# Performance work log

Hardware: AMD Instinct MI355X
Metric: run time of the kernel (lower is better)

## Reference

```python
import jax, jax.numpy as jnp
import numpy as np

FP8_MAX = 448.0   # E4M3 max finite value
AMAX_EPS = 1e-8
MOMENTUM = 0.95


def _compute_scale(amax):
    return FP8_MAX / jnp.clip(amax, AMAX_EPS)


def _fp8_cast_ste(t, scale):
    """clamp(t*scale, +-448) -> fp8_e4m3 -> back to t.dtype, /scale. STE grad."""
    s = scale.astype(jnp.float32)
    t_scaled = jnp.clip(t.astype(jnp.float32) * s, -FP8_MAX, FP8_MAX)
    t_deq = t_scaled.astype(jnp.float8_e4m3fn).astype(t.dtype) / s.astype(t.dtype)
    # straight-through: forward value = t_deq, gradient = identity wrt t
    return t + jax.lax.stop_gradient(t_deq - t)


def _update_amax(buf, new_amax):
    new_amax = jnp.nan_to_num(new_amax, nan=AMAX_EPS, posinf=FP8_MAX, neginf=AMAX_EPS)
    return jnp.clip(jnp.maximum(buf * MOMENTUM, new_amax), AMAX_EPS)


def setup_inputs() -> dict:
    key = jax.random.key(0)
    k1, k2, k3 = jax.random.split(key, 3)
    x = jax.random.normal(k1, (8192, 4096), dtype=jnp.float32)
    weight = jax.random.normal(k2, (4096, 4096), dtype=jnp.float32) * 0.02
    bias = jax.random.normal(k3, (4096,), dtype=jnp.float32) * 0.01
    input_amax = jnp.ones((), dtype=jnp.float32)
    weight_amax = jnp.ones((), dtype=jnp.float32)
    return {"x": x, "weight": weight, "bias": bias,
            "input_amax": input_amax, "weight_amax": weight_amax}


def reference(x, weight, bias, input_amax, weight_amax):
    # delayed scaling: scales from previous-step amax buffers
    x_scale = _compute_scale(input_amax).astype(jnp.float32)
    w_scale = _compute_scale(weight_amax).astype(jnp.float32)
    x2 = x.reshape(-1, weight.shape[1])  # [T, in]
    x_q = _fp8_cast_ste(x2, x_scale)
    w_q = _fp8_cast_ste(weight, w_scale)
    out = jnp.einsum('ti,oi->to', x_q, w_q) + bias  # [T, out]
    # amax EMA updates (buffers)
    new_input_amax = _update_amax(input_amax, jnp.max(jnp.abs(x2)))
    new_weight_amax = _update_amax(weight_amax, jnp.max(jnp.abs(weight)))
    return out, new_input_amax, new_weight_amax
```

## Files before the change

### kernel.cpp

```cpp
#include <hip/hip_runtime.h>
#include <cstdint>
#include <cstddef>

#define FP8_MAXV 448.0f
#define AMAX_EPS 1e-8f
#define MOMENTUM 0.95f

#define M_DIM 8192
#define N_DIM 4096
#define K_DIM 4096

#define XBLOCKS 2048
#define WBLOCKS 1024

#define SCALE_ONE 0x7F7F7F7F

typedef float f32x4 __attribute__((ext_vector_type(4)));
typedef int   i32x4 __attribute__((ext_vector_type(4)));
typedef int   i32x8 __attribute__((ext_vector_type(8)));

__device__ __forceinline__ void gload_lds16(const void* g, void* l) {
  __builtin_amdgcn_global_load_lds(
      (const __attribute__((address_space(1))) void*)g,
      (__attribute__((address_space(3))) void*)l, 16, 0, 0);
}

__global__ __launch_bounds__(256) void k_quant(
    const float* __restrict__ x, const float* __restrict__ w,
    unsigned int* __restrict__ xq, unsigned int* __restrict__ wq,
    const float* __restrict__ ax_buf, const float* __restrict__ aw_buf,
    float* __restrict__ xpart, float* __restrict__ wpart) {
  const float* in;
  unsigned int* outq;
  float* part;
  int bid, nblocks, n4;
  float sc;
  if (blockIdx.x < XBLOCKS) {
    in = x; outq = xq; part = xpart;
    bid = blockIdx.x; nblocks = XBLOCKS; n4 = (M_DIM * K_DIM) / 4;
    sc = FP8_MAXV / fmaxf(ax_buf[0], AMAX_EPS);
  } else {
    in = w; outq = wq; part = wpart;
    bid = blockIdx.x - XBLOCKS; nblocks = WBLOCKS; n4 = (N_DIM * K_DIM) / 4;
    sc = FP8_MAXV / fmaxf(aw_buf[0], AMAX_EPS);
  }
  float lm = 0.0f;
  const int stride = nblocks * 256;
  for (int i = bid * 256 + threadIdx.x; i < n4; i += stride) {
    float4 v = ((const float4*)in)[i];
    lm = fmaxf(lm, fmaxf(fmaxf(fabsf(v.x), fabsf(v.y)),
                         fmaxf(fabsf(v.z), fabsf(v.w))));
    float a0 = fminf(fmaxf(v.x * sc, -FP8_MAXV), FP8_MAXV);
    float a1 = fminf(fmaxf(v.y * sc, -FP8_MAXV), FP8_MAXV);
    float a2 = fminf(fmaxf(v.z * sc, -FP8_MAXV), FP8_MAXV);
    float a3 = fminf(fmaxf(v.w * sc, -FP8_MAXV), FP8_MAXV);
    int p = 0;
    p = __builtin_amdgcn_cvt_pk_fp8_f32(a0, a1, p, false);
    p = __builtin_amdgcn_cvt_pk_fp8_f32(a2, a3, p, true);
    outq[i] = (unsigned int)p;
  }
  #pragma unroll
  for (int off = 32; off > 0; off >>= 1)
    lm = fmaxf(lm, __shfl_down(lm, off));
  __shared__ float smax[4];
  if ((threadIdx.x & 63) == 0) smax[threadIdx.x >> 6] = lm;
  __syncthreads();
  if (threadIdx.x == 0)
    part[bid] = fmaxf(fmaxf(smax[0], smax[1]), fmaxf(smax[2], smax[3]));
}

__global__ __launch_bounds__(256, 2) void k_gemm(
    const unsigned char* __restrict__ Aq, const unsigned char* __restrict__ Bq,
    const float* __restrict__ bias,
    const float* __restrict__ ax_buf, const float* __restrict__ aw_buf,
    const float* __restrict__ xpart, const float* __restrict__ wpart,
    float* __restrict__ out) {
  __shared__ __align__(16) unsigned char ldsA[128 * 128];
  __shared__ __align__(16) unsigned char ldsB[128 * 128];

  const int tid = threadIdx.x;
  const int w = tid >> 6;
  const int l = tid & 63;
  const int m = l & 15;
  const int q = l >> 4;
  const int wr = (w >> 1) * 64;
  const int wc = (w & 1) * 64;
  const int blockRow = blockIdx.y * 128;
  const int blockCol = blockIdx.x * 128;

  const int srow = l >> 3;
  const int sgrp = (l & 7) ^ srow;
  const unsigned char* gA =
      Aq + (size_t)(blockRow + w * 32 + srow) * K_DIM + sgrp * 16;
  const unsigned char* gB =
      Bq + (size_t)(blockCol + w * 32 + srow) * K_DIM + sgrp * 16;
  unsigned char* lA = &ldsA[w * 4096];
  unsigned char* lB = &ldsB[w * 4096];

  const int mk = m & 7;
  f32x4 acc[4][4] = {};

  for (int k0 = 0; k0 < K_DIM; k0 += 128) {
    #pragma unroll
    for (int cc = 0; cc < 4; ++cc) {
      gload_lds16(gA + k0 + (size_t)(cc * 8) * K_DIM, lA + cc * 1024);
      gload_lds16(gB + k0 + (size_t)(cc * 8) * K_DIM, lB + cc * 1024);
    }
    __syncthreads();

    i32x8 a[4], b[4];
    #pragma unroll
    for (int i = 0; i < 4; ++i) {
      const unsigned char* p = ldsA + (wr + i * 16 + m) * 128;
      i32x4 lo = *(const i32x4*)(p + (((2 * q) ^ mk) * 16));
      i32x4 hi = *(const i32x4*)(p + (((2 * q + 1) ^ mk) * 16));
      a[i] = __builtin_shufflevector(lo, hi, 0, 1, 2, 3, 4, 5, 6, 7);
    }
    #pragma unroll
    for (int j = 0; j < 4; ++j) {
      const unsigned char* p = ldsB + (wc + j * 16 + m) * 128;
      i32x4 lo = *(const i32x4*)(p + (((2 * q) ^ mk) * 16));
      i32x4 hi = *(const i32x4*)(p + (((2 * q + 1) ^ mk) * 16));
      b[j] = __builtin_shufflevector(lo, hi, 0, 1, 2, 3, 4, 5, 6, 7);
    }
    #pragma unroll
    for (int i = 0; i < 4; ++i)
      #pragma unroll
      for (int j = 0; j < 4; ++j)
        acc[i][j] = __builtin_amdgcn_mfma_scale_f32_16x16x128_f8f6f4(
            a[i], b[j], acc[i][j],  0,  0,
             0, SCALE_ONE,  0, SCALE_ONE);
    __syncthreads();
  }

  const float inv = fmaxf(ax_buf[0], AMAX_EPS) * fmaxf(aw_buf[0], AMAX_EPS) *
                    (1.0f / (FP8_MAXV * FP8_MAXV));

  #pragma unroll
  for (int j = 0; j < 4; ++j) {
    const int colg = blockCol + wc + j * 16 + m;
    const float bv = bias[colg];
    #pragma unroll
    for (int i = 0; i < 4; ++i) {
      const int rowg = blockRow + wr + i * 16 + q * 4;
      #pragma unroll
      for (int r = 0; r < 4; ++r)
        out[(size_t)(rowg + r) * N_DIM + colg] = acc[i][j][r] * inv + bv;
    }
  }

  if (blockIdx.x == 0 && blockIdx.y == 0) {
    float mx = 0.0f, mw = 0.0f;
    for (int i = tid; i < XBLOCKS; i += 256) mx = fmaxf(mx, xpart[i]);
    for (int i = tid; i < WBLOCKS; i += 256) mw = fmaxf(mw, wpart[i]);
    #pragma unroll
    for (int off = 32; off > 0; off >>= 1) {
      mx = fmaxf(mx, __shfl_down(mx, off));
      mw = fmaxf(mw, __shfl_down(mw, off));
    }
    __syncthreads();
    float* red = (float*)ldsA;
    if (l == 0) { red[w] = mx; red[4 + w] = mw; }
    __syncthreads();
    if (tid == 0) {
      mx = fmaxf(fmaxf(red[0], red[1]), fmaxf(red[2], red[3]));
      mw = fmaxf(fmaxf(red[4], red[5]), fmaxf(red[6], red[7]));
      float* tail = out + (size_t)M_DIM * N_DIM;
      tail[0] = fmaxf(fmaxf(ax_buf[0] * MOMENTUM, mx), AMAX_EPS);
      tail[1] = fmaxf(fmaxf(aw_buf[0] * MOMENTUM, mw), AMAX_EPS);
    }
  }
}

extern "C" void kernel_launch(void* const* d_in, const int* in_sizes, int n_in,
                              void* d_out, int out_size, void* d_ws, size_t ws_size,
                              hipStream_t stream) {
  const float* x      = (const float*)d_in[0];
  const float* weight = (const float*)d_in[1];
  const float* bias   = (const float*)d_in[2];
  const float* in_ax  = (const float*)d_in[3];
  const float* in_aw  = (const float*)d_in[4];
  float* out = (float*)d_out;

  float* xpart = (float*)d_ws;
  float* wpart = xpart + XBLOCKS;
  unsigned char* xq = (unsigned char*)d_ws + 16384;
  unsigned char* wq = xq + (size_t)M_DIM * K_DIM;

  k_quant<<<XBLOCKS + WBLOCKS, 256, 0, stream>>>(
      x, weight, (unsigned int*)xq, (unsigned int*)wq, in_ax, in_aw,
      xpart, wpart);

  dim3 grid(N_DIM / 128, M_DIM / 128);
  k_gemm<<<grid, 256, 0, stream>>>(xq, wq, bias, in_ax, in_aw,
                                   xpart, wpart, out);
}
```

Baseline: 408.3 us.

## Enlarge GEMM tile to 256x256 with double-buffered LDS and interleaved MFMA

The FP8 GEMM goes from a 128x128 tile with 4 waves to a 256x256 tile with 8 waves, each wave computing 128x64. LDS is double buffered so the next K-slab's global-to-LDS loads are issued before the current slab's MFMAs run. Fragment reads are interleaved with MFMA pairs under s_setprio. This aims to raise operand reuse and hide load latency behind compute, at the cost of 128KB of LDS per block and heavy register pressure from 32 accumulators, which may limit occupancy.

```diff
diff --git a/kernel.cpp b/kernel.cpp
--- a/kernel.cpp
+++ b/kernel.cpp
@@ -69,68 +69,110 @@
     part[bid] = fmaxf(fmaxf(smax[0], smax[1]), fmaxf(smax[2], smax[3]));
 }
 
-__global__ __launch_bounds__(256, 2) void k_gemm(
+__global__ __launch_bounds__(512, 2) void k_gemm(
     const unsigned char* __restrict__ Aq, const unsigned char* __restrict__ Bq,
     const float* __restrict__ bias,
     const float* __restrict__ ax_buf, const float* __restrict__ aw_buf,
     const float* __restrict__ xpart, const float* __restrict__ wpart,
     float* __restrict__ out) {
-  __shared__ __align__(16) unsigned char ldsA[128 * 128];
-  __shared__ __align__(16) unsigned char ldsB[128 * 128];
+  __shared__ __align__(16) unsigned char ldsA[2][256 * 128];
+  __shared__ __align__(16) unsigned char ldsB[2][256 * 128];
 
   const int tid = threadIdx.x;
   const int w = tid >> 6;
   const int l = tid & 63;
   const int m = l & 15;
   const int q = l >> 4;
-  const int wr = (w >> 1) * 64;
-  const int wc = (w & 1) * 64;
-  const int blockRow = blockIdx.y * 128;
-  const int blockCol = blockIdx.x * 128;
+  const int mk = m & 7;
+  const int wr = (w >> 2) * 128;
+  const int wc = (w & 3) * 64;
+  const int blockRow = blockIdx.y * 256;
+  const int blockCol = blockIdx.x * 256;
+
+  const int xlo = ((2 * q) ^ mk) * 16;
+  const int xhi = ((2 * q + 1) ^ mk) * 16;
 
   const int srow = l >> 3;
-  const int sgrp = (l & 7) ^ srow;
-  const unsigned char* gA =
-      Aq + (size_t)(blockRow + w * 32 + srow) * K_DIM + sgrp * 16;
-  const unsigned char* gB =
-      Bq + (size_t)(blockCol + w * 32 + srow) * K_DIM + sgrp * 16;
-  unsigned char* lA = &ldsA[w * 4096];
-  unsigned char* lB = &ldsB[w * 4096];
-
-  const int mk = m & 7;
-  f32x4 acc[4][4] = {};
-
-  for (int k0 = 0; k0 < K_DIM; k0 += 128) {
+  const int sgrp = ((l & 7) ^ srow) * 16;
+  const unsigned char* gA = Aq + (size_t)(blockRow + w * 32 + srow) * K_DIM + sgrp;
+  const unsigned char* gB = Bq + (size_t)(blockCol + w * 32 + srow) * K_DIM + sgrp;
+
+#define STAGE(bufidx, k0)                                              \
+  { _Pragma("unroll") for (int s = 0; s < 4; ++s) {                    \
+      gload_lds16(gA + (k0) + (size_t)(s * 8) * K_DIM,                 \
+                  &ldsA[bufidx][w * 4096 + s * 1024]);                 \
+      gload_lds16(gB + (k0) + (size_t)(s * 8) * K_DIM,                 \
+                  &ldsB[bufidx][w * 4096 + s * 1024]);                 \
+  } }
+
+#define FRAG2(lo, hi, off)                                             \
+  __builtin_shufflevector(*(const i32x4*)((lo) + (off)),               \
+                          *(const i32x4*)((hi) + (off)), 0, 1, 2, 3, 4, 5, 6, 7)
+
+#define MFMA_PAIR(i0, aX, aY)                                          \
+  { __builtin_amdgcn_s_setprio(1);                                     \
+    _Pragma("unroll") for (int j = 0; j < 4; ++j) {                    \
+      acc[(i0)][j] = __builtin_amdgcn_mfma_scale_f32_16x16x128_f8f6f4( \
+          aX, b[j], acc[(i0)][j], 0, 0, 0, SCALE_ONE, 0, SCALE_ONE);   \
+      acc[(i0) + 1][j] = __builtin_amdgcn_mfma_scale_f32_16x16x128_f8f6f4( \
+          aY, b[j], acc[(i0) + 1][j], 0, 0, 0, SCALE_ONE, 0, SCALE_ONE);   \
+    }                                                                  \
+    __builtin_amdgcn_s_setprio(0); }
+
+  f32x4 acc[8][4] = {};
+  const int NT = K_DIM / 128;
+
+  STAGE(0, 0);
+  asm volatile("s_waitcnt vmcnt(0)" ::: "memory");
+  __builtin_amdgcn_s_barrier();
+
+  i32x8 b[4], a0f, a1f;
+  {
+    const unsigned char* Blo = &ldsB[0][(wc + m) * 128 + xlo];
+    const unsigned char* Bhi = &ldsB[0][(wc + m) * 128 + xhi];
+    const unsigned char* Alo = &ldsA[0][(wr + m) * 128 + xlo];
+    const unsigned char* Ahi = &ldsA[0][(wr + m) * 128 + xhi];
     #pragma unroll
-    for (int cc = 0; cc < 4; ++cc) {
-      gload_lds16(gA + k0 + (size_t)(cc * 8) * K_DIM, lA + cc * 1024);
-      gload_lds16(gB + k0 + (size_t)(cc * 8) * K_DIM, lB + cc * 1024);
-    }
-    __syncthreads();
-
-    i32x8 a[4], b[4];
-    #pragma unroll
-    for (int i = 0; i < 4; ++i) {
-      const unsigned char* p = ldsA + (wr + i * 16 + m) * 128;
-      i32x4 lo = *(const i32x4*)(p + (((2 * q) ^ mk) * 16));
-      i32x4 hi = *(const i32x4*)(p + (((2 * q + 1) ^ mk) * 16));
-      a[i] = __builtin_shufflevector(lo, hi, 0, 1, 2, 3, 4, 5, 6, 7);
-    }
-    #pragma unroll
-    for (int j = 0; j < 4; ++j) {
-      const unsigned char* p = ldsB + (wc + j * 16 + m) * 128;
-      i32x4 lo = *(const i32x4*)(p + (((2 * q) ^ mk) * 16));
-      i32x4 hi = *(const i32x4*)(p + (((2 * q + 1) ^ mk) * 16));
-      b[j] = __builtin_shufflevector(lo, hi, 0, 1, 2, 3, 4, 5, 6, 7);
-    }
-    #pragma unroll
-    for (int i = 0; i < 4; ++i)
+    for (int j = 0; j < 4; ++j) b[j] = FRAG2(Blo, Bhi, j * 2048);
+    a0f = FRAG2(Alo, Ahi, 0);
+    a1f = FRAG2(Alo, Ahi, 2048);
+  }
+
+  for (int kt = 0; kt < NT; ++kt) {
+    const int cur = kt & 1;
+    const unsigned char* Alo = &ldsA[cur][(wr + m) * 128 + xlo];
+    const unsigned char* Ahi = &ldsA[cur][(wr + m) * 128 + xhi];
+
+    if (kt + 1 < NT) STAGE(cur ^ 1, (kt + 1) * 128);
+    MFMA_PAIR(0, a0f, a1f);
+    i32x8 a2f = FRAG2(Alo, Ahi, 2 * 2048);
+    i32x8 a3f = FRAG2(Alo, Ahi, 3 * 2048);
+    __builtin_amdgcn_s_barrier();
+
+    MFMA_PAIR(2, a2f, a3f);
+    i32x8 a4f = FRAG2(Alo, Ahi, 4 * 2048);
+    i32x8 a5f = FRAG2(Alo, Ahi, 5 * 2048);
+    __builtin_amdgcn_s_barrier();
+
+    MFMA_PAIR(4, a4f, a5f);
+    i32x8 a6f = FRAG2(Alo, Ahi, 6 * 2048);
+    i32x8 a7f = FRAG2(Alo, Ahi, 7 * 2048);
+    asm volatile("s_waitcnt vmcnt(0)" ::: "memory");
+    __builtin_amdgcn_s_barrier();
+
+    MFMA_PAIR(6, a6f, a7f);
+    if (kt + 1 < NT) {
+      const int nxt = cur ^ 1;
+      const unsigned char* Bnlo = &ldsB[nxt][(wc + m) * 128 + xlo];
+      const unsigned char* Bnhi = &ldsB[nxt][(wc + m) * 128 + xhi];
+      const unsigned char* Anlo = &ldsA[nxt][(wr + m) * 128 + xlo];
+      const unsigned char* Anhi = &ldsA[nxt][(wr + m) * 128 + xhi];
       #pragma unroll
-      for (int j = 0; j < 4; ++j)
-        acc[i][j] = __builtin_amdgcn_mfma_scale_f32_16x16x128_f8f6f4(
-            a[i], b[j], acc[i][j],  0,  0,
-             0, SCALE_ONE,  0, SCALE_ONE);
-    __syncthreads();
+      for (int j = 0; j < 4; ++j) b[j] = FRAG2(Bnlo, Bnhi, j * 2048);
+      a0f = FRAG2(Anlo, Anhi, 0);
+      a1f = FRAG2(Anlo, Anhi, 2048);
+    }
+    __builtin_amdgcn_s_barrier();
   }
 
   const float inv = fmaxf(ax_buf[0], AMAX_EPS) * fmaxf(aw_buf[0], AMAX_EPS) *
@@ -141,7 +183,7 @@
     const int colg = blockCol + wc + j * 16 + m;
     const float bv = bias[colg];
     #pragma unroll
-    for (int i = 0; i < 4; ++i) {
+    for (int i = 0; i < 8; ++i) {
       const int rowg = blockRow + wr + i * 16 + q * 4;
       #pragma unroll
       for (int r = 0; r < 4; ++r)
@@ -151,8 +193,8 @@
 
   if (blockIdx.x == 0 && blockIdx.y == 0) {
     float mx = 0.0f, mw = 0.0f;
-    for (int i = tid; i < XBLOCKS; i += 256) mx = fmaxf(mx, xpart[i]);
-    for (int i = tid; i < WBLOCKS; i += 256) mw = fmaxf(mw, wpart[i]);
+    for (int i = tid; i < XBLOCKS; i += 512) mx = fmaxf(mx, xpart[i]);
+    for (int i = tid; i < WBLOCKS; i += 512) mw = fmaxf(mw, wpart[i]);
     #pragma unroll
     for (int off = 32; off > 0; off >>= 1) {
       mx = fmaxf(mx, __shfl_down(mx, off));
@@ -160,11 +202,15 @@
     }
     __syncthreads();
     float* red = (float*)ldsA;
-    if (l == 0) { red[w] = mx; red[4 + w] = mw; }
+    if (l == 0) { red[w] = mx; red[8 + w] = mw; }
     __syncthreads();
     if (tid == 0) {
-      mx = fmaxf(fmaxf(red[0], red[1]), fmaxf(red[2], red[3]));
-      mw = fmaxf(fmaxf(red[4], red[5]), fmaxf(red[6], red[7]));
+      mx = red[0]; mw = red[8];
+      #pragma unroll
+      for (int i = 1; i < 8; ++i) {
+        mx = fmaxf(mx, red[i]);
+        mw = fmaxf(mw, red[8 + i]);
+      }
       float* tail = out + (size_t)M_DIM * N_DIM;
       tail[0] = fmaxf(fmaxf(ax_buf[0] * MOMENTUM, mx), AMAX_EPS);
       tail[1] = fmaxf(fmaxf(aw_buf[0] * MOMENTUM, mw), AMAX_EPS);
@@ -191,7 +237,7 @@
       x, weight, (unsigned int*)xq, (unsigned int*)wq, in_ax, in_aw,
       xpart, wpart);
 
-  dim3 grid(N_DIM / 128, M_DIM / 128);
-  k_gemm<<<grid, 256, 0, stream>>>(xq, wq, bias, in_ax, in_aw,
+  dim3 grid(N_DIM / 256, M_DIM / 256);
+  k_gemm<<<grid, 512, 0, stream>>>(xq, wq, bias, in_ax, in_aw,
                                    xpart, wpart, out);
 }
```

After: 410.6 us. No clear change (+0.6%).
